# Kernel tuning notes

Measured on AMD Instinct MI355X. Metric: run time of the kernel, lower is better.

## Reference

```python
import jax, jax.numpy as jnp
from jax import lax
import numpy as np

B, T, I, H, O = 128, 256, 256, 1024, 128


def _rnn_layer(x, W_ih, W_hh, b_ih, b_hh):
    # x: [B, T, D_in] -> hidden states [B, T, H]
    # precompute input projection for all timesteps (batched GEMM)
    xW = jnp.einsum('btd,hd->bth', x, W_ih) + b_ih + b_hh  # [B, T, H]

    def step(h, xw_t):
        h = jnp.tanh(xw_t + h @ W_hh.T)  # [B, H]
        return h, h

    h0 = jnp.zeros((x.shape[0], W_hh.shape[0]), x.dtype)
    _, hs = lax.scan(step, h0, jnp.swapaxes(xW, 0, 1))  # hs: [T, B, H]
    return jnp.swapaxes(hs, 0, 1)  # [B, T, H]


def setup_inputs() -> dict:
    key = jax.random.key(0)
    ks = jax.random.split(key, 11)
    s_ih0 = 1.0 / np.sqrt(H)
    inp = {
        'X': jax.random.normal(ks[0], (B, T, I), jnp.float32),
        'W_ih0': jax.random.uniform(ks[1], (H, I), jnp.float32, -s_ih0, s_ih0),
        'W_hh0': jax.random.uniform(ks[2], (H, H), jnp.float32, -s_ih0, s_ih0),
        'b_ih0': jax.random.uniform(ks[3], (H,), jnp.float32, -s_ih0, s_ih0),
        'b_hh0': jax.random.uniform(ks[4], (H,), jnp.float32, -s_ih0, s_ih0),
        'W_ih1': jax.random.uniform(ks[5], (H, H), jnp.float32, -s_ih0, s_ih0),
        'W_hh1': jax.random.uniform(ks[6], (H, H), jnp.float32, -s_ih0, s_ih0),
        'b_ih1': jax.random.uniform(ks[7], (H,), jnp.float32, -s_ih0, s_ih0),
        'b_hh1': jax.random.uniform(ks[8], (H,), jnp.float32, -s_ih0, s_ih0),
        'W_fc': jax.random.uniform(ks[9], (O, H), jnp.float32, -s_ih0, s_ih0),
        'b_fc': jax.random.uniform(ks[10], (O,), jnp.float32, -s_ih0, s_ih0),
    }
    return inp


def reference(X, W_ih0, W_hh0, b_ih0, b_hh0, W_ih1, W_hh1, b_ih1, b_hh1, W_fc, b_fc):
    h1 = _rnn_layer(X, W_ih0, W_hh0, b_ih0, b_hh0)   # layer 0: [B, T, H]
    h2 = _rnn_layer(h1, W_ih1, W_hh1, b_ih1, b_hh1)  # layer 1: [B, T, H]
    last = h2[:, -1, :]                               # [B, H]
    return last @ W_fc.T + b_fc                       # [B, O]
```

## Files before the change

kernel.cpp:

```cpp
#include <hip/hip_runtime.h>
#include <stdint.h>
#include <stddef.h>

#define B_ 128
#define T_ 256
#define I_ 256
#define H_ 1024
#define O_ 128

typedef __attribute__((ext_vector_type(8))) __bf16 bf16x8;
typedef __attribute__((ext_vector_type(4))) float f32x4;
typedef unsigned long long u64;



__global__ void split_kernel(const float* __restrict__ src, __bf16* __restrict__ hi,
                             __bf16* __restrict__ lo, int n) {
    int i = blockIdx.x * blockDim.x + threadIdx.x;
    int stride = gridDim.x * blockDim.x;
    for (; i < n; i += stride) {
        float v = src[i];
        __bf16 h = (__bf16)v;
        hi[i] = h;
        lo[i] = (__bf16)(v - (float)h);
    }
}

__global__ void pack_x(const float* __restrict__ X, u64* __restrict__ xp) {
    int i = blockIdx.x * 256 + threadIdx.x;
    int ln = i & 15;
    int k2 = (i >> 4) & 127;
    int bt16 = (i >> 11) & 7;
    int t = i >> 14;
    int b = bt16 * 16 + ln;
    long xo = (long)b * T_ * I_ + (long)t * I_ + k2 * 2;
    float v0 = X[xo], v1 = X[xo + 1];
    union { __bf16 b; unsigned short u; } h0, l0, h1, l1;
    h0.b = (__bf16)v0; l0.b = (__bf16)(v0 - (float)h0.b);
    h1.b = (__bf16)v1; l1.b = (__bf16)(v1 - (float)h1.b);
    u64 pk = (u64)((unsigned)h0.u | ((unsigned)l0.u << 16))
           | ((u64)((unsigned)h1.u | ((unsigned)l1.u << 16)) << 32);
    xp[(long)t * 16384 + bt16 * 2048 + k2 * 16 + ln] = pk;
}

__global__ void bias_sum_kernel(const float* __restrict__ a, const float* __restrict__ b,
                                float* __restrict__ o, int n) {
    int i = blockIdx.x * blockDim.x + threadIdx.x;
    if (i < n) o[i] = a[i] + b[i];
}

__global__ void transpose_fc(const float* __restrict__ w, float* __restrict__ wt) {
    int i = blockIdx.x * blockDim.x + threadIdx.x;
    if (i < O_ * H_) {
        int o = i / H_, k = i - o * H_;
        wt[k * O_ + o] = w[i];
    }
}


__device__ __forceinline__ void unpack4(const u64* d, bf16x8* hi, bf16x8* lo) {
    union { unsigned u[4]; bf16x8 v; } Hh, Ll;
    #pragma unroll
    for (int i = 0; i < 4; ++i) {
        unsigned lo32 = (unsigned)d[i], hi32 = (unsigned)(d[i] >> 32);
        Hh.u[i] = (lo32 & 0xFFFFu) | (hi32 << 16);
        Ll.u[i] = (lo32 >> 16) | (hi32 & 0xFFFF0000u);
    }
    *hi = Hh.v; *lo = Ll.v;
}

__device__ __forceinline__ void load_swz(const u64* p, bf16x8* hi, bf16x8* lo) {
    u64 d[4];
    #pragma unroll
    for (int i = 0; i < 4; ++i)
        d[i] = __hip_atomic_load((u64*)p + i * 16, __ATOMIC_RELAXED,
                                 __HIP_MEMORY_SCOPE_AGENT);
    unpack4(d, hi, lo);
}

__device__ __forceinline__ void load_swz_cached(const u64* p, bf16x8* hi, bf16x8* lo) {
    u64 d[4];
    #pragma unroll
    for (int i = 0; i < 4; ++i)
        d[i] = p[i * 16];
    unpack4(d, hi, lo);
}

template <int CPW, int SEG0CH, bool CACHED0>
__device__ __forceinline__ void step_full(
    const u64* __restrict__ A0,
    const u64* __restrict__ Sp,
    const bf16x8 (&wh)[CPW][2], const bf16x8 (&wl)[CPW][2],
    const float* __restrict__ bs,
    u64* __restrict__ So, u64* __restrict__ Qo,
    int bt, int jt, int w, float* red)
{
    const int lane = threadIdx.x & 63;
    const int ln = lane & 15;
    const int q  = lane >> 4;

    f32x4 acc[2][2][3];
    #pragma unroll
    for (int s = 0; s < 2; ++s)
        #pragma unroll
        for (int n = 0; n < 2; ++n)
            #pragma unroll
            for (int r = 0; r < 3; ++r)
                acc[s][n][r] = (f32x4){0.f, 0.f, 0.f, 0.f};

    #pragma unroll
    for (int c = 0; c < CPW; ++c) {
        int gC = w * CPW + c;
        bf16x8 ah[2], al[2];
        if (gC < SEG0CH) {
            const u64* base = A0 + (long)(gC * 16 + q * 4) * 16 + ln;
            #pragma unroll
            for (int s = 0; s < 2; ++s) {
                const u64* p = base + (long)(bt * 2 + s) * (SEG0CH * 256);
                if (CACHED0) load_swz_cached(p, &ah[s], &al[s]);
                else         load_swz(p, &ah[s], &al[s]);
            }
        } else {
            const u64* base = Sp + (long)((gC - SEG0CH) * 16 + q * 4) * 16 + ln;
            #pragma unroll
            for (int s = 0; s < 2; ++s)
                load_swz(base + (long)(bt * 2 + s) * 8192, &ah[s], &al[s]);
        }
        #pragma unroll
        for (int s = 0; s < 2; ++s)
            #pragma unroll
            for (int n = 0; n < 2; ++n) {
                acc[s][n][0] = __builtin_amdgcn_mfma_f32_16x16x32_bf16(ah[s], wh[c][n], acc[s][n][0], 0, 0, 0);
                acc[s][n][1] = __builtin_amdgcn_mfma_f32_16x16x32_bf16(al[s], wh[c][n], acc[s][n][1], 0, 0, 0);
                acc[s][n][2] = __builtin_amdgcn_mfma_f32_16x16x32_bf16(ah[s], wl[c][n], acc[s][n][2], 0, 0, 0);
            }
    }

    {
        float* my = red + w * 1056;
        #pragma unroll
        for (int s = 0; s < 2; ++s)
            #pragma unroll
            for (int n = 0; n < 2; ++n) {
                f32x4 sum = acc[s][n][0] + acc[s][n][1] + acc[s][n][2];
                #pragma unroll
                for (int r = 0; r < 4; ++r)
                    my[(s * 16 + q * 4 + r) * 33 + n * 16 + ln] = sum[r];
            }
    }
    __syncthreads();

    {
        int tid = threadIdx.x;
        int row = tid & 31;
        int jp  = tid >> 5;
        int c0 = jp * 2;
        float v0 = 0.f, v1 = 0.f;
        #pragma unroll
        for (int w8 = 0; w8 < 8; ++w8) {
            v0 += red[w8 * 1056 + row * 33 + c0];
            v1 += red[w8 * 1056 + row * 33 + c0 + 1];
        }
        int j0 = jt * 32 + c0;
        float h0 = tanhf(v0 + bs[j0]);
        float h1v = tanhf(v1 + bs[j0 + 1]);
        union { __bf16 b; unsigned short u; } x0h, x0l, x1h, x1l;
        x0h.b = (__bf16)h0;  x0l.b = (__bf16)(h0 - (float)x0h.b);
        x1h.b = (__bf16)h1v; x1l.b = (__bf16)(h1v - (float)x1h.b);
        u64 pk = (u64)((unsigned)x0h.u | ((unsigned)x0l.u << 16))
               | ((u64)((unsigned)x1h.u | ((unsigned)x1l.u << 16)) << 32);
        long idx = (long)(bt * 2 + (row >> 4)) * 8192 + (long)(jt * 16 + jp) * 16 + (row & 15);
        __hip_atomic_store(&So[idx], pk, __ATOMIC_RELAXED, __HIP_MEMORY_SCOPE_AGENT);
        if (Qo)
            __hip_atomic_store(&Qo[idx], pk, __ATOMIC_RELAXED, __HIP_MEMORY_SCOPE_AGENT);
    }
}

__device__ __forceinline__ void grid_barrier(unsigned* bar, int grp, unsigned step) {
    asm volatile("s_waitcnt vmcnt(0)" ::: "memory");
    __syncthreads();
    if (threadIdx.x == 0) {
        unsigned tgt = step + 1u;
        unsigned old = __hip_atomic_fetch_add(&bar[grp * 32], 1u, __ATOMIC_RELAXED,
                                              __HIP_MEMORY_SCOPE_AGENT);
        if ((old & 31u) == 31u) {
            unsigned so = __hip_atomic_fetch_add(&bar[256], 1u, __ATOMIC_RELAXED,
                                                 __HIP_MEMORY_SCOPE_AGENT);
            if ((so & 7u) == 7u) {
                #pragma unroll
                for (int i = 0; i < 8; ++i)
                    __hip_atomic_store(&bar[512 + i * 32], tgt, __ATOMIC_RELAXED,
                                       __HIP_MEMORY_SCOPE_AGENT);
            }
        }
        while (__hip_atomic_load(&bar[512 + grp * 32], __ATOMIC_RELAXED,
                                 __HIP_MEMORY_SCOPE_AGENT) < tgt)
            __builtin_amdgcn_s_sleep(2);
    }
    __syncthreads();
    asm volatile("" ::: "memory");
}

struct PArgs {
    const u64* xp;
    const __bf16 *Wi0h, *Wi0l, *Wr0h, *Wr0l;
    const __bf16 *Wi1h, *Wi1l, *Wr1h, *Wr1l;
    const float *bs0, *bs1;
    u64 *h1;
    u64 *s0a, *s0b, *s1a, *s1b;
    unsigned* bar;
};

__global__ __launch_bounds__(512, 2) void persistent_rnn(PArgs a) {
    __shared__ float red[8 * 1056];
    const int w = threadIdx.x >> 6;
    const int lane = threadIdx.x & 63;
    const int ln = lane & 15;
    const int q  = lane >> 4;
    const int grp = blockIdx.x & 7;
    const int layer = blockIdx.x >> 7;
    const int r7 = blockIdx.x & 127;
    const int jt = r7 & 31;
    const int bt = r7 >> 5;

    if (layer == 0) {
        bf16x8 wh[5][2], wl[5][2];
        #pragma unroll
        for (int c = 0; c < 5; ++c) {
            int gC = w * 5 + c;
            #pragma unroll
            for (int n = 0; n < 2; ++n) {
                int jr = jt * 32 + n * 16 + ln;
                if (gC < 8) {
                    wh[c][n] = *(const bf16x8*)(a.Wi0h + (long)jr * 256 + gC * 32 + q * 8);
                    wl[c][n] = *(const bf16x8*)(a.Wi0l + (long)jr * 256 + gC * 32 + q * 8);
                } else {
                    wh[c][n] = *(const bf16x8*)(a.Wr0h + (long)jr * 1024 + (gC - 8) * 32 + q * 8);
                    wl[c][n] = *(const bf16x8*)(a.Wr0l + (long)jr * 1024 + (gC - 8) * 32 + q * 8);
                }
            }
        }
        for (int t = 0; t <= T_; ++t) {
            if (t < T_) {
                const u64* sin = (t & 1) ? a.s0b : a.s0a;
                u64* sout      = (t & 1) ? a.s0a : a.s0b;
                step_full<5, 8, true>(a.xp + (long)t * 16384, sin, wh, wl, a.bs0,
                                      sout, a.h1 + (long)t * 65536, bt, jt, w, red);
            }
            grid_barrier(a.bar, grp, (unsigned)t);
        }
    } else {
        bf16x8 wh[8][2], wl[8][2];
        #pragma unroll
        for (int c = 0; c < 8; ++c) {
            int gC = w * 8 + c;
            #pragma unroll
            for (int n = 0; n < 2; ++n) {
                int jr = jt * 32 + n * 16 + ln;
                if (gC < 32) {
                    wh[c][n] = *(const bf16x8*)(a.Wi1h + (long)jr * 1024 + gC * 32 + q * 8);
                    wl[c][n] = *(const bf16x8*)(a.Wi1l + (long)jr * 1024 + gC * 32 + q * 8);
                } else {
                    wh[c][n] = *(const bf16x8*)(a.Wr1h + (long)jr * 1024 + (gC - 32) * 32 + q * 8);
                    wl[c][n] = *(const bf16x8*)(a.Wr1l + (long)jr * 1024 + (gC - 32) * 32 + q * 8);
                }
            }
        }
        for (int t = 0; t <= T_; ++t) {
            if (t >= 1) {
                int t1 = t - 1;
                const u64* sin = (t1 & 1) ? a.s1b : a.s1a;
                u64* sout      = (t1 & 1) ? a.s1a : a.s1b;
                step_full<8, 32, false>(a.h1 + (long)t1 * 65536, sin, wh, wl, a.bs1,
                                        sout, (u64*)nullptr, bt, jt, w, red);
            }
            grid_barrier(a.bar, grp, (unsigned)t);
        }
    }
}

__global__ __launch_bounds__(128) void fc_kernel(const u64* __restrict__ sp,
                                                 const float* __restrict__ wt,
                                                 const float* __restrict__ bfc,
                                                 float* __restrict__ out) {
    int b = blockIdx.x;
    int o = threadIdx.x;
    int bt = b >> 4, r = b & 15;
    float acc = 0.f;
    #pragma unroll 4
    for (int k2 = 0; k2 < H_ / 2; ++k2) {
        u64 pk = __hip_atomic_load((u64*)sp + (long)bt * 8192 + (long)k2 * 16 + r,
                                   __ATOMIC_RELAXED, __HIP_MEMORY_SCOPE_AGENT);
        union { unsigned short u; __bf16 bf; } hh, hl;
        unsigned lo32 = (unsigned)pk, hi32 = (unsigned)(pk >> 32);
        hh.u = (unsigned short)(lo32 & 0xFFFF); hl.u = (unsigned short)(lo32 >> 16);
        float x0 = (float)hh.bf + (float)hl.bf;
        hh.u = (unsigned short)(hi32 & 0xFFFF); hl.u = (unsigned short)(hi32 >> 16);
        float x1 = (float)hh.bf + (float)hl.bf;
        acc += x0 * wt[(2 * k2) * O_ + o] + x1 * wt[(2 * k2 + 1) * O_ + o];
    }
    out[b * O_ + o] = acc + bfc[o];
}


extern "C" void kernel_launch(void* const* d_in, const int* in_sizes, int n_in,
                              void* d_out, int out_size, void* d_ws, size_t ws_size,
                              hipStream_t stream) {
    const float* X     = (const float*)d_in[0];
    const float* Wih0  = (const float*)d_in[1];
    const float* Whh0  = (const float*)d_in[2];
    const float* bih0  = (const float*)d_in[3];
    const float* bhh0  = (const float*)d_in[4];
    const float* Wih1  = (const float*)d_in[5];
    const float* Whh1  = (const float*)d_in[6];
    const float* bih1  = (const float*)d_in[7];
    const float* bhh1  = (const float*)d_in[8];
    const float* Wfc   = (const float*)d_in[9];
    const float* bfc   = (const float*)d_in[10];
    float* out = (float*)d_out;

    char* p = (char*)d_ws;
    auto alloc = [&](size_t bytes) -> void* {
        void* r = (void*)p;
        p += (bytes + 255) & ~(size_t)255;
        return r;
    };
    const size_t nW0 = (size_t)H_ * I_;
    const size_t nW  = (size_t)H_ * H_;
    u64* xp      = (u64*)alloc((size_t)T_ * 16384 * 8);
    __bf16* W0h  = (__bf16*)alloc(nW0 * 2);
    __bf16* W0l  = (__bf16*)alloc(nW0 * 2);
    __bf16* Wh0h = (__bf16*)alloc(nW * 2);
    __bf16* Wh0l = (__bf16*)alloc(nW * 2);
    __bf16* Wi1h = (__bf16*)alloc(nW * 2);
    __bf16* Wi1l = (__bf16*)alloc(nW * 2);
    __bf16* Wh1h = (__bf16*)alloc(nW * 2);
    __bf16* Wh1l = (__bf16*)alloc(nW * 2);
    u64* h1   = (u64*)alloc((size_t)T_ * 65536 * 8);
    u64* s0a  = (u64*)alloc(65536 * 8);
    u64* s0b  = (u64*)alloc(65536 * 8);
    u64* s1a  = (u64*)alloc(65536 * 8);
    u64* s1b  = (u64*)alloc(65536 * 8);
    float* wfct = (float*)alloc((size_t)H_ * O_ * 4);
    float* bs0  = (float*)alloc((size_t)H_ * 4);
    float* bs1  = (float*)alloc((size_t)H_ * 4);
    unsigned* bar = (unsigned*)alloc(4096);
    (void)ws_size; (void)n_in; (void)in_sizes; (void)out_size;

    pack_x<<<16384, 256, 0, stream>>>(X, xp);
    split_kernel<<<512, 256, 0, stream>>>(Wih0, W0h, W0l, (int)nW0);
    split_kernel<<<1024, 256, 0, stream>>>(Whh0, Wh0h, Wh0l, (int)nW);
    split_kernel<<<1024, 256, 0, stream>>>(Wih1, Wi1h, Wi1l, (int)nW);
    split_kernel<<<1024, 256, 0, stream>>>(Whh1, Wh1h, Wh1l, (int)nW);
    bias_sum_kernel<<<4, 256, 0, stream>>>(bih0, bhh0, bs0, H_);
    bias_sum_kernel<<<4, 256, 0, stream>>>(bih1, bhh1, bs1, H_);
    transpose_fc<<<(O_ * H_ + 255) / 256, 256, 0, stream>>>(Wfc, wfct);

    hipMemsetAsync(s0a, 0, 65536 * 8, stream);
    hipMemsetAsync(s1a, 0, 65536 * 8, stream);
    hipMemsetAsync(bar, 0, 4096, stream);

    PArgs args;
    args.xp = xp;
    args.Wi0h = W0h; args.Wi0l = W0l; args.Wr0h = Wh0h; args.Wr0l = Wh0l;
    args.Wi1h = Wi1h; args.Wi1l = Wi1l; args.Wr1h = Wh1h; args.Wr1l = Wh1l;
    args.bs0 = bs0; args.bs1 = bs1;
    args.h1 = h1;
    args.s0a = s0a; args.s0b = s0b; args.s1a = s1a; args.s1b = s1b;
    args.bar = bar;
    void* kp[] = { &args };
    hipLaunchCooperativeKernel((void*)persistent_rnn, dim3(256), dim3(512), kp, 0, stream);

    fc_kernel<<<B_, O_, 0, stream>>>(s1a, wfct, bfc, out);
}
```

Before: 2.187 ms.

## Drop activation lo-split to single bf16 and decouple layer barriers into cohorts

```diff
diff --git a/kernel.cpp b/kernel.cpp
--- a/kernel.cpp
+++ b/kernel.cpp
@@ -11,6 +11,7 @@
 typedef __attribute__((ext_vector_type(8))) __bf16 bf16x8;
 typedef __attribute__((ext_vector_type(4))) float f32x4;
 typedef unsigned long long u64;
+typedef unsigned int u32;
 
 
 
@@ -26,21 +27,21 @@
     }
 }
 
-__global__ void pack_x(const float* __restrict__ X, u64* __restrict__ xp) {
+__global__ void pack_x(const float* __restrict__ X, u32* __restrict__ xp) {
     int i = blockIdx.x * 256 + threadIdx.x;
-    int ln = i & 15;
-    int k2 = (i >> 4) & 127;
+    int dw   = i & 3;
+    int ln   = (i >> 2) & 15;
+    int k8   = (i >> 6) & 31;
     int bt16 = (i >> 11) & 7;
-    int t = i >> 14;
+    int t    = i >> 14;
+    int k = k8 * 8 + dw * 2;
     int b = bt16 * 16 + ln;
-    long xo = (long)b * T_ * I_ + (long)t * I_ + k2 * 2;
-    float v0 = X[xo], v1 = X[xo + 1];
-    union { __bf16 b; unsigned short u; } h0, l0, h1, l1;
-    h0.b = (__bf16)v0; l0.b = (__bf16)(v0 - (float)h0.b);
-    h1.b = (__bf16)v1; l1.b = (__bf16)(v1 - (float)h1.b);
-    u64 pk = (u64)((unsigned)h0.u | ((unsigned)l0.u << 16))
-           | ((u64)((unsigned)h1.u | ((unsigned)l1.u << 16)) << 32);
-    xp[(long)t * 16384 + bt16 * 2048 + k2 * 16 + ln] = pk;
+    long xo = (long)b * T_ * I_ + (long)t * I_ + k;
+    union { __bf16 b; unsigned short u; } h0, h1;
+    h0.b = (__bf16)X[xo];
+    h1.b = (__bf16)X[xo + 1];
+    xp[(long)t * 16384 + bt16 * 2048 + k8 * 64 + ln * 4 + dw] =
+        (u32)h0.u | ((u32)h1.u << 16);
 }
 
 __global__ void bias_sum_kernel(const float* __restrict__ a, const float* __restrict__ b,
@@ -58,81 +59,72 @@
 }
 
 
-__device__ __forceinline__ void unpack4(const u64* d, bf16x8* hi, bf16x8* lo) {
-    union { unsigned u[4]; bf16x8 v; } Hh, Ll;
-    #pragma unroll
-    for (int i = 0; i < 4; ++i) {
-        unsigned lo32 = (unsigned)d[i], hi32 = (unsigned)(d[i] >> 32);
-        Hh.u[i] = (lo32 & 0xFFFFu) | (hi32 << 16);
-        Ll.u[i] = (lo32 >> 16) | (hi32 & 0xFFFF0000u);
-    }
-    *hi = Hh.v; *lo = Ll.v;
-}
-
-__device__ __forceinline__ void load_swz(const u64* p, bf16x8* hi, bf16x8* lo) {
-    u64 d[4];
-    #pragma unroll
-    for (int i = 0; i < 4; ++i)
-        d[i] = __hip_atomic_load((u64*)p + i * 16, __ATOMIC_RELAXED,
-                                 __HIP_MEMORY_SCOPE_AGENT);
-    unpack4(d, hi, lo);
-}
-
-__device__ __forceinline__ void load_swz_cached(const u64* p, bf16x8* hi, bf16x8* lo) {
-    u64 d[4];
-    #pragma unroll
-    for (int i = 0; i < 4; ++i)
-        d[i] = p[i * 16];
-    unpack4(d, hi, lo);
-}
-
-template <int CPW, int SEG0CH, bool CACHED0>
+__device__ __forceinline__ bf16x8 load_frag_sc1(const u64* p) {
+    union { u64 d[2]; bf16x8 v; } r;
+    r.d[0] = __hip_atomic_load((u64*)p,     __ATOMIC_RELAXED, __HIP_MEMORY_SCOPE_AGENT);
+    r.d[1] = __hip_atomic_load((u64*)p + 1, __ATOMIC_RELAXED, __HIP_MEMORY_SCOPE_AGENT);
+    return r.v;
+}
+
+template <int CPW, int SEG0CH, bool X0>
 __device__ __forceinline__ void step_full(
-    const u64* __restrict__ A0,
+    const u32* __restrict__ xA0,
+    const u64* __restrict__ hA0,
     const u64* __restrict__ Sp,
     const bf16x8 (&wh)[CPW][2], const bf16x8 (&wl)[CPW][2],
     const float* __restrict__ bs,
-    u64* __restrict__ So, u64* __restrict__ Qo,
+    u32* __restrict__ So, u32* __restrict__ Qo,
     int bt, int jt, int w, float* red)
 {
     const int lane = threadIdx.x & 63;
     const int ln = lane & 15;
     const int q  = lane >> 4;
 
-    f32x4 acc[2][2][3];
+    f32x4 acc[2][2][2];
     #pragma unroll
     for (int s = 0; s < 2; ++s)
         #pragma unroll
         for (int n = 0; n < 2; ++n)
             #pragma unroll
-            for (int r = 0; r < 3; ++r)
+            for (int r = 0; r < 2; ++r)
                 acc[s][n][r] = (f32x4){0.f, 0.f, 0.f, 0.f};
 
     #pragma unroll
     for (int c = 0; c < CPW; ++c) {
         int gC = w * CPW + c;
-        bf16x8 ah[2], al[2];
+        bf16x8 ah[2];
         if (gC < SEG0CH) {
-            const u64* base = A0 + (long)(gC * 16 + q * 4) * 16 + ln;
+            if (X0) {
+                #pragma unroll
+                for (int s = 0; s < 2; ++s) {
+                    long off = (long)(bt * 2 + s) * (SEG0CH * 256)
+                             + (gC * 4 + q) * 64 + ln * 4;
+                    union { uint4 u; bf16x8 v; } r;
+                    r.u = *(const uint4*)(xA0 + off);
+                    ah[s] = r.v;
+                }
+            } else {
+                #pragma unroll
+                for (int s = 0; s < 2; ++s) {
+                    long idx = (long)(bt * 2 + s) * (SEG0CH * 128)
+                             + (gC * 4 + q) * 32 + ln * 2;
+                    ah[s] = load_frag_sc1(hA0 + idx);
+                }
+            }
+        } else {
             #pragma unroll
             for (int s = 0; s < 2; ++s) {
-                const u64* p = base + (long)(bt * 2 + s) * (SEG0CH * 256);
-                if (CACHED0) load_swz_cached(p, &ah[s], &al[s]);
-                else         load_swz(p, &ah[s], &al[s]);
-            }
-        } else {
-            const u64* base = Sp + (long)((gC - SEG0CH) * 16 + q * 4) * 16 + ln;
-            #pragma unroll
-            for (int s = 0; s < 2; ++s)
-                load_swz(base + (long)(bt * 2 + s) * 8192, &ah[s], &al[s]);
+                long idx = (long)(bt * 2 + s) * 4096
+                         + ((gC - SEG0CH) * 4 + q) * 32 + ln * 2;
+                ah[s] = load_frag_sc1(Sp + idx);
+            }
         }
         #pragma unroll
         for (int s = 0; s < 2; ++s)
             #pragma unroll
             for (int n = 0; n < 2; ++n) {
                 acc[s][n][0] = __builtin_amdgcn_mfma_f32_16x16x32_bf16(ah[s], wh[c][n], acc[s][n][0], 0, 0, 0);
-                acc[s][n][1] = __builtin_amdgcn_mfma_f32_16x16x32_bf16(al[s], wh[c][n], acc[s][n][1], 0, 0, 0);
-                acc[s][n][2] = __builtin_amdgcn_mfma_f32_16x16x32_bf16(ah[s], wl[c][n], acc[s][n][2], 0, 0, 0);
+                acc[s][n][1] = __builtin_amdgcn_mfma_f32_16x16x32_bf16(ah[s], wl[c][n], acc[s][n][1], 0, 0, 0);
             }
     }
 
@@ -142,7 +134,7 @@
         for (int s = 0; s < 2; ++s)
             #pragma unroll
             for (int n = 0; n < 2; ++n) {
-                f32x4 sum = acc[s][n][0] + acc[s][n][1] + acc[s][n][2];
+                f32x4 sum = acc[s][n][0] + acc[s][n][1];
                 #pragma unroll
                 for (int r = 0; r < 4; ++r)
                     my[(s * 16 + q * 4 + r) * 33 + n * 16 + ln] = sum[r];
@@ -164,36 +156,44 @@
         int j0 = jt * 32 + c0;
         float h0 = tanhf(v0 + bs[j0]);
         float h1v = tanhf(v1 + bs[j0 + 1]);
-        union { __bf16 b; unsigned short u; } x0h, x0l, x1h, x1l;
-        x0h.b = (__bf16)h0;  x0l.b = (__bf16)(h0 - (float)x0h.b);
-        x1h.b = (__bf16)h1v; x1l.b = (__bf16)(h1v - (float)x1h.b);
-        u64 pk = (u64)((unsigned)x0h.u | ((unsigned)x0l.u << 16))
-               | ((u64)((unsigned)x1h.u | ((unsigned)x1l.u << 16)) << 32);
-        long idx = (long)(bt * 2 + (row >> 4)) * 8192 + (long)(jt * 16 + jp) * 16 + (row & 15);
-        __hip_atomic_store(&So[idx], pk, __ATOMIC_RELAXED, __HIP_MEMORY_SCOPE_AGENT);
+        union { __bf16 b; unsigned short u; } a0, a1;
+        a0.b = (__bf16)h0;
+        a1.b = (__bf16)h1v;
+        u32 pk = (u32)a0.u | ((u32)a1.u << 16);
+        int bgrp = bt * 2 + (row >> 4);
+        long uidx = (long)bgrp * 8192 + (jt * 4 + (jp >> 2)) * 64
+                  + (row & 15) * 4 + (jp & 3);
+        __hip_atomic_store(&So[uidx], pk, __ATOMIC_RELAXED, __HIP_MEMORY_SCOPE_AGENT);
         if (Qo)
-            __hip_atomic_store(&Qo[idx], pk, __ATOMIC_RELAXED, __HIP_MEMORY_SCOPE_AGENT);
-    }
-}
-
-__device__ __forceinline__ void grid_barrier(unsigned* bar, int grp, unsigned step) {
+            __hip_atomic_store(&Qo[uidx], pk, __ATOMIC_RELAXED, __HIP_MEMORY_SCOPE_AGENT);
+    }
+}
+
+__device__ __forceinline__ void cohort_barrier(unsigned* bar, int cohort, int grp,
+                                               unsigned tgt, bool pub_prog) {
     asm volatile("s_waitcnt vmcnt(0)" ::: "memory");
     __syncthreads();
     if (threadIdx.x == 0) {
-        unsigned tgt = step + 1u;
-        unsigned old = __hip_atomic_fetch_add(&bar[grp * 32], 1u, __ATOMIC_RELAXED,
+        unsigned* base = bar + cohort * 1024;
+        unsigned old = __hip_atomic_fetch_add(&base[grp * 32], 1u, __ATOMIC_RELAXED,
                                               __HIP_MEMORY_SCOPE_AGENT);
-        if ((old & 31u) == 31u) {
-            unsigned so = __hip_atomic_fetch_add(&bar[256], 1u, __ATOMIC_RELAXED,
+        if ((old & 15u) == 15u) {
+            unsigned so = __hip_atomic_fetch_add(&base[256], 1u, __ATOMIC_RELAXED,
                                                  __HIP_MEMORY_SCOPE_AGENT);
             if ((so & 7u) == 7u) {
                 #pragma unroll
-                for (int i = 0; i < 8; ++i)
-                    __hip_atomic_store(&bar[512 + i * 32], tgt, __ATOMIC_RELAXED,
+                for (int g = 0; g < 8; ++g)
+                    __hip_atomic_store(&base[512 + g * 32], tgt, __ATOMIC_RELAXED,
                                        __HIP_MEMORY_SCOPE_AGENT);
-            }
-        }
-        while (__hip_atomic_load(&bar[512 + grp * 32], __ATOMIC_RELAXED,
+                if (pub_prog) {
+                    #pragma unroll
+                    for (int g = 0; g < 8; ++g)
+                        __hip_atomic_store(&bar[2048 + g * 32], tgt, __ATOMIC_RELAXED,
+                                           __HIP_MEMORY_SCOPE_AGENT);
+                }
+            }
+        }
+        while (__hip_atomic_load(&base[512 + grp * 32], __ATOMIC_RELAXED,
                                  __HIP_MEMORY_SCOPE_AGENT) < tgt)
             __builtin_amdgcn_s_sleep(2);
     }
@@ -202,12 +202,12 @@
 }
 
 struct PArgs {
-    const u64* xp;
+    const u32* xp;
     const __bf16 *Wi0h, *Wi0l, *Wr0h, *Wr0l;
     const __bf16 *Wi1h, *Wi1l, *Wr1h, *Wr1l;
     const float *bs0, *bs1;
-    u64 *h1;
-    u64 *s0a, *s0b, *s1a, *s1b;
+    u32 *h1;
+    u32 *s0a, *s0b, *s1a, *s1b;
     unsigned* bar;
 };
 
@@ -217,9 +217,9 @@
     const int lane = threadIdx.x & 63;
     const int ln = lane & 15;
     const int q  = lane >> 4;
-    const int grp = blockIdx.x & 7;
     const int layer = blockIdx.x >> 7;
     const int r7 = blockIdx.x & 127;
+    const int grp = r7 & 7;
     const int jt = r7 & 31;
     const int bt = r7 >> 5;
 
@@ -240,14 +240,13 @@
                 }
             }
         }
-        for (int t = 0; t <= T_; ++t) {
-            if (t < T_) {
-                const u64* sin = (t & 1) ? a.s0b : a.s0a;
-                u64* sout      = (t & 1) ? a.s0a : a.s0b;
-                step_full<5, 8, true>(a.xp + (long)t * 16384, sin, wh, wl, a.bs0,
-                                      sout, a.h1 + (long)t * 65536, bt, jt, w, red);
-            }
-            grid_barrier(a.bar, grp, (unsigned)t);
+        for (int t = 0; t < T_; ++t) {
+            const u32* sin = (t & 1) ? a.s0b : a.s0a;
+            u32* sout      = (t & 1) ? a.s0a : a.s0b;
+            step_full<5, 8, true>(a.xp + (long)t * 16384, (const u64*)nullptr,
+                                  (const u64*)sin, wh, wl, a.bs0,
+                                  sout, a.h1 + (long)t * 65536, bt, jt, w, red);
+            cohort_barrier(a.bar, 0, grp, (unsigned)(t + 1), true);
         }
     } else {
         bf16x8 wh[8][2], wl[8][2];
@@ -266,38 +265,40 @@
                 }
             }
         }
-        for (int t = 0; t <= T_; ++t) {
-            if (t >= 1) {
-                int t1 = t - 1;
-                const u64* sin = (t1 & 1) ? a.s1b : a.s1a;
-                u64* sout      = (t1 & 1) ? a.s1a : a.s1b;
-                step_full<8, 32, false>(a.h1 + (long)t1 * 65536, sin, wh, wl, a.bs1,
-                                        sout, (u64*)nullptr, bt, jt, w, red);
-            }
-            grid_barrier(a.bar, grp, (unsigned)t);
-        }
-    }
-}
-
-__global__ __launch_bounds__(128) void fc_kernel(const u64* __restrict__ sp,
+        for (int t1 = 0; t1 < T_; ++t1) {
+            if (threadIdx.x == 0) {
+                while (__hip_atomic_load(&a.bar[2048 + grp * 32], __ATOMIC_RELAXED,
+                                         __HIP_MEMORY_SCOPE_AGENT) < (unsigned)(t1 + 1))
+                    __builtin_amdgcn_s_sleep(2);
+            }
+            __syncthreads();
+            const u32* sin = (t1 & 1) ? a.s1b : a.s1a;
+            u32* sout      = (t1 & 1) ? a.s1a : a.s1b;
+            step_full<8, 32, false>((const u32*)nullptr,
+                                    (const u64*)(a.h1 + (long)t1 * 65536),
+                                    (const u64*)sin, wh, wl, a.bs1,
+                                    sout, (u32*)nullptr, bt, jt, w, red);
+            cohort_barrier(a.bar, 1, grp, (unsigned)(t1 + 1), false);
+        }
+    }
+}
+
+__global__ __launch_bounds__(128) void fc_kernel(const u32* __restrict__ sp,
                                                  const float* __restrict__ wt,
                                                  const float* __restrict__ bfc,
                                                  float* __restrict__ out) {
     int b = blockIdx.x;
     int o = threadIdx.x;
-    int bt = b >> 4, r = b & 15;
+    int bgrp = b >> 4, ln = b & 15;
     float acc = 0.f;
     #pragma unroll 4
-    for (int k2 = 0; k2 < H_ / 2; ++k2) {
-        u64 pk = __hip_atomic_load((u64*)sp + (long)bt * 8192 + (long)k2 * 16 + r,
-                                   __ATOMIC_RELAXED, __HIP_MEMORY_SCOPE_AGENT);
-        union { unsigned short u; __bf16 bf; } hh, hl;
-        unsigned lo32 = (unsigned)pk, hi32 = (unsigned)(pk >> 32);
-        hh.u = (unsigned short)(lo32 & 0xFFFF); hl.u = (unsigned short)(lo32 >> 16);
-        float x0 = (float)hh.bf + (float)hl.bf;
-        hh.u = (unsigned short)(hi32 & 0xFFFF); hl.u = (unsigned short)(hi32 >> 16);
-        float x1 = (float)hh.bf + (float)hl.bf;
-        acc += x0 * wt[(2 * k2) * O_ + o] + x1 * wt[(2 * k2 + 1) * O_ + o];
+    for (int kp = 0; kp < H_ / 2; ++kp) {
+        u32 v = sp[(long)bgrp * 8192 + (kp >> 2) * 64 + ln * 4 + (kp & 3)];
+        union { unsigned short u; __bf16 bf; } e0, e1;
+        e0.u = (unsigned short)(v & 0xFFFF);
+        e1.u = (unsigned short)(v >> 16);
+        acc += (float)e0.bf * wt[(2 * kp) * O_ + o]
+             + (float)e1.bf * wt[(2 * kp + 1) * O_ + o];
     }
     out[b * O_ + o] = acc + bfc[o];
 }
@@ -327,7 +328,7 @@
     };
     const size_t nW0 = (size_t)H_ * I_;
     const size_t nW  = (size_t)H_ * H_;
-    u64* xp      = (u64*)alloc((size_t)T_ * 16384 * 8);
+    u32* xp      = (u32*)alloc((size_t)T_ * 16384 * 4);
     __bf16* W0h  = (__bf16*)alloc(nW0 * 2);
     __bf16* W0l  = (__bf16*)alloc(nW0 * 2);
     __bf16* Wh0h = (__bf16*)alloc(nW * 2);
@@ -336,15 +337,15 @@
     __bf16* Wi1l = (__bf16*)alloc(nW * 2);
     __bf16* Wh1h = (__bf16*)alloc(nW * 2);
     __bf16* Wh1l = (__bf16*)alloc(nW * 2);
-    u64* h1   = (u64*)alloc((size_t)T_ * 65536 * 8);
-    u64* s0a  = (u64*)alloc(65536 * 8);
-    u64* s0b  = (u64*)alloc(65536 * 8);
-    u64* s1a  = (u64*)alloc(65536 * 8);
-    u64* s1b  = (u64*)alloc(65536 * 8);
+    u32* h1   = (u32*)alloc((size_t)T_ * 65536 * 4);
+    u32* s0a  = (u32*)alloc(65536 * 4);
+    u32* s0b  = (u32*)alloc(65536 * 4);
+    u32* s1a  = (u32*)alloc(65536 * 4);
+    u32* s1b  = (u32*)alloc(65536 * 4);
     float* wfct = (float*)alloc((size_t)H_ * O_ * 4);
     float* bs0  = (float*)alloc((size_t)H_ * 4);
     float* bs1  = (float*)alloc((size_t)H_ * 4);
-    unsigned* bar = (unsigned*)alloc(4096);
+    unsigned* bar = (unsigned*)alloc(16384);
     (void)ws_size; (void)n_in; (void)in_sizes; (void)out_size;
 
     pack_x<<<16384, 256, 0, stream>>>(X, xp);
@@ -356,9 +357,9 @@
     bias_sum_kernel<<<4, 256, 0, stream>>>(bih1, bhh1, bs1, H_);
     transpose_fc<<<(O_ * H_ + 255) / 256, 256, 0, stream>>>(Wfc, wfct);
 
-    hipMemsetAsync(s0a, 0, 65536 * 8, stream);
-    hipMemsetAsync(s1a, 0, 65536 * 8, stream);
-    hipMemsetAsync(bar, 0, 4096, stream);
+    hipMemsetAsync(s0a, 0, 65536 * 4, stream);
+    hipMemsetAsync(s1a, 0, 65536 * 4, stream);
+    hipMemsetAsync(bar, 0, 16384, stream);
 
     PArgs args;
     args.xp = xp;
```

After: 2.257 ms. 3.2% more time.
